# Performance work log

Hardware: AMD Instinct MI355X
Metric: run time of the kernel (lower is better)

## Reference

```python
import jax, jax.numpy as jnp
import numpy as np

N, IN_C, OUT_C, FEAT_C, G = 1_000_000, 64, 64, 128, 4096


def setup_inputs() -> dict:
    key = jax.random.key(0)
    ks = jax.random.split(key, 9)
    x = jax.random.normal(ks[0], (N, IN_C), dtype=jnp.float32)
    origin_feat = jax.random.normal(ks[1], (G, FEAT_C), dtype=jnp.float32)
    latent_point_batch = jax.random.randint(ks[2], (N,), 0, G, dtype=jnp.int32)
    s_fc = 1.0 / np.sqrt(IN_C)
    s_ft = 1.0 / np.sqrt(FEAT_C)
    W_fc = jax.random.uniform(ks[3], (IN_C, OUT_C), jnp.float32, -s_fc, s_fc)
    b_fc = jax.random.uniform(ks[4], (OUT_C,), jnp.float32, -s_fc, s_fc)
    W_mu = jax.random.uniform(ks[5], (FEAT_C, OUT_C), jnp.float32, -s_ft, s_ft)
    b_mu = jax.random.uniform(ks[6], (OUT_C,), jnp.float32, -s_ft, s_ft)
    W_sig = jax.random.uniform(ks[7], (FEAT_C, OUT_C), jnp.float32, -s_ft, s_ft)
    b_sig = jax.random.uniform(ks[8], (OUT_C,), jnp.float32, -s_ft, s_ft)
    return {"x": x, "origin_feat": origin_feat, "latent_point_batch": latent_point_batch,
            "num_groups": G, "W_fc": W_fc, "b_fc": b_fc, "W_mu": W_mu, "b_mu": b_mu,
            "W_sig": W_sig, "b_sig": b_sig}


def _segment_mean(v, seg, num_segments):
    # [N, C] -> [G, C] per-segment mean
    s = jax.ops.segment_sum(v, seg, num_segments=num_segments)
    cnt = jax.ops.segment_sum(jnp.ones((v.shape[0],), v.dtype), seg,
                              num_segments=num_segments)
    return s / jnp.maximum(cnt, 1.0)[:, None]


def reference(x, origin_feat, latent_point_batch, num_groups,
              W_fc, b_fc, W_mu, b_mu, W_sig, b_sig):
    h = x @ W_fc + b_fc                      # [N, outC]
    mu = origin_feat @ W_mu + b_mu           # [G, outC]
    sig = origin_feat @ W_sig + b_sig        # [G, outC]
    seg = latent_point_batch
    h_mean = _segment_mean(h, seg, num_groups)          # [G, outC]
    h_c = h - h_mean[seg]                                # centered
    h_var = _segment_mean(h_c * h_c, seg, num_groups)    # biased var per group
    h_n = h_c / jnp.sqrt(h_var[seg] + 1e-14)
    out = jax.nn.relu(h_n * sig[seg] + mu[seg])
    return out
```

## Files before the change

kernel.cpp:

```cpp
#include <hip/hip_runtime.h>
#include <hip/hip_bf16.h>
#include <stdint.h>

typedef unsigned int u32;
typedef unsigned short u16;

__device__ __forceinline__ float bf2f(u32 b) {
  union { u32 u; float f; } v; v.u = b << 16; return v.f;
}

__global__ void FCAdaINLayer_68719477052_kernel(const u16* __restrict__ xb,
                                                int* __restrict__ cnt, int G,
                                                int* __restrict__ flag) {
  int t = blockIdx.x * blockDim.x + threadIdx.x;
  int stride = gridDim.x * blockDim.x;
  for (int i = t; i < G; i += stride) cnt[i] = 0;
  if (blockIdx.x == 0 && threadIdx.x < 64) {
    int lane = threadIdx.x;
    int big = 0;
    for (int j = lane; j < 2048; j += 64) {
      u32 e = ((u32)xb[j] >> 7) & 0xffu;
      if (e >= 140u) big++;
    }
    unsigned long long m = __ballot(big > 0);
    if (lane == 0) *flag = (__popcll(m) > 8) ? 1 : 0;
  }
}

__global__ void k_hist(const int* __restrict__ lat, int n, int* __restrict__ cnt) {
  int i = blockIdx.x * blockDim.x + threadIdx.x;
  int stride = gridDim.x * blockDim.x;
  for (; i < n; i += stride) atomicAdd(&cnt[lat[i]], 1);
}

__global__ void k_scan(const int* __restrict__ cnt, int G, int* __restrict__ offs,
                       int* __restrict__ cursor) {
  __shared__ int part[256];
  int t = threadIdx.x;
  int per = (G + 255) / 256;
  int base = t * per;
  int s = 0;
  for (int j = 0; j < per; j++) { int g = base + j; if (g < G) s += cnt[g]; }
  part[t] = s;
  __syncthreads();
  if (t == 0) {
    int run = 0;
    for (int j = 0; j < 256; j++) { int v = part[j]; part[j] = run; run += v; }
  }
  __syncthreads();
  int run = part[t];
  for (int j = 0; j < per; j++) {
    int g = base + j;
    if (g < G) { offs[g] = run; cursor[g] = run; run += cnt[g]; }
  }
  if (t == 255) offs[G] = run;
}

__global__ void k_scatter(const int* __restrict__ lat, int n, int* __restrict__ cursor,
                          int* __restrict__ sorted) {
  int i = blockIdx.x * blockDim.x + threadIdx.x;
  int stride = gridDim.x * blockDim.x;
  for (; i < n; i += stride) {
    int g = lat[i];
    int pos = atomicAdd(&cursor[g], 1);
    sorted[pos] = i;
  }
}

template <bool F32>
__global__ void k_musig(const void* __restrict__ of, const void* __restrict__ Wmu,
                        const void* __restrict__ bmu, const void* __restrict__ Wsig,
                        const void* __restrict__ bsig, const int* __restrict__ flag,
                        float* __restrict__ mug, float* __restrict__ sgg, int total) {
  if ((*flag != 0) != F32) return;
  int idx = blockIdx.x * blockDim.x + threadIdx.x;
  if (idx >= total) return;
  int g = idx >> 6, c = idx & 63;
  float a0 = 0.f, a1 = 0.f, bm, bs;
  if (F32) {
    const float* ofr = (const float*)of + (size_t)g * 128;
    const float* wm = (const float*)Wmu;
    const float* wsv = (const float*)Wsig;
    for (int k = 0; k < 128; k++) {
      float ov = ofr[k];
      a0 = fmaf(ov, wm[k * 64 + c], a0);
      a1 = fmaf(ov, wsv[k * 64 + c], a1);
    }
    bm = ((const float*)bmu)[c];
    bs = ((const float*)bsig)[c];
  } else {
    const u16* ofr = (const u16*)of + (size_t)g * 128;
    const u16* wm = (const u16*)Wmu;
    const u16* wsv = (const u16*)Wsig;
    for (int k = 0; k < 128; k++) {
      float ov = bf2f((u32)ofr[k]);
      a0 = fmaf(ov, bf2f((u32)wm[k * 64 + c]), a0);
      a1 = fmaf(ov, bf2f((u32)wsv[k * 64 + c]), a1);
    }
    bm = bf2f((u32)((const u16*)bmu)[c]);
    bs = bf2f((u32)((const u16*)bsig)[c]);
  }
  mug[idx] = a0 + bm;
  sgg[idx] = a1 + bs;
}

__device__ __forceinline__ float h_bf16(const uint4* __restrict__ xr,
                                        const float* wcol, float bc) {
  float h0 = bc, h1 = 0.f, h2 = 0.f, h3 = 0.f;
#pragma unroll
  for (int j = 0; j < 8; j++) {
    uint4 q = xr[j];
    u32 qs[4] = {q.x, q.y, q.z, q.w};
#pragma unroll
    for (int m = 0; m < 4; m++) {
      float flo = __uint_as_float(qs[m] << 16);
      float fhi = __uint_as_float(qs[m] & 0xffff0000u);
      int k = j * 8 + m * 2;
      if ((m & 1) == 0) { h0 = fmaf(flo, wcol[k], h0); h1 = fmaf(fhi, wcol[k + 1], h1); }
      else             { h2 = fmaf(flo, wcol[k], h2); h3 = fmaf(fhi, wcol[k + 1], h3); }
    }
  }
  return (h0 + h2) + (h1 + h3);
}

__device__ __forceinline__ float h_f32(const float4* __restrict__ xr,
                                       const float* wcol, float bc) {
  float h0 = bc, h1 = 0.f, h2 = 0.f, h3 = 0.f;
#pragma unroll
  for (int j = 0; j < 16; j++) {
    float4 q = xr[j];
    int k = j * 4;
    h0 = fmaf(q.x, wcol[k], h0);
    h1 = fmaf(q.y, wcol[k + 1], h1);
    h2 = fmaf(q.z, wcol[k + 2], h2);
    h3 = fmaf(q.w, wcol[k + 3], h3);
  }
  return (h0 + h2) + (h1 + h3);
}

template <bool F32>
__global__ void k_main(const void* __restrict__ x, const int* __restrict__ sorted,
                       const int* __restrict__ offs, const float* __restrict__ mug,
                       const float* __restrict__ sgg, const void* __restrict__ Wfc,
                       const void* __restrict__ bfc, const int* __restrict__ flag,
                       void* __restrict__ out) {
  if ((*flag != 0) != F32) return;
  int g = blockIdx.x;
  int lane = threadIdx.x & 63;
  int wid = threadIdx.x >> 6;
  int beg = offs[g], end = offs[g + 1];
  int cnt = end - beg;
  if (cnt == 0) return;
  __shared__ float red[2][4][64];

  float wcol[64];
  float bc;
  if (F32) {
    const float* W = (const float*)Wfc;
#pragma unroll
    for (int k = 0; k < 64; k++) wcol[k] = W[k * 64 + lane];
    bc = ((const float*)bfc)[lane];
  } else {
    const u16* W = (const u16*)Wfc;
#pragma unroll
    for (int k = 0; k < 64; k++) wcol[k] = bf2f((u32)W[k * 64 + lane]);
    bc = bf2f((u32)((const u16*)bfc)[lane]);
  }

  float ssum = 0.f, ssq = 0.f;
  for (int i = beg + wid; i < end; i += 4) {
    int p = __builtin_amdgcn_readfirstlane(sorted[i]);
    float h;
    if (F32) h = h_f32(reinterpret_cast<const float4*>(x) + (size_t)p * 16, wcol, bc);
    else     h = h_bf16(reinterpret_cast<const uint4*>(x) + (size_t)p * 8, wcol, bc);
    ssum += h;
    ssq = fmaf(h, h, ssq);
  }
  red[0][wid][lane] = ssum;
  red[1][wid][lane] = ssq;
  __syncthreads();
  float ts = 0.f, tq = 0.f;
#pragma unroll
  for (int w = 0; w < 4; w++) { ts += red[0][w][lane]; tq += red[1][w][lane]; }
  float inv = 1.0f / (float)cnt;
  float mean = ts * inv;
  float var = fmaxf(tq * inv - mean * mean, 0.f);
  float rstd = rsqrtf(var + 1e-14f);
  float scale = sgg[(size_t)g * 64 + lane] * rstd;
  float shift = mug[(size_t)g * 64 + lane] - mean * scale;

  for (int i = beg + wid; i < end; i += 4) {
    int p = __builtin_amdgcn_readfirstlane(sorted[i]);
    float h;
    if (F32) h = h_f32(reinterpret_cast<const float4*>(x) + (size_t)p * 16, wcol, bc);
    else     h = h_bf16(reinterpret_cast<const uint4*>(x) + (size_t)p * 8, wcol, bc);
    float o = fmaxf(fmaf(h, scale, shift), 0.f);
    if (F32) ((float*)out)[(size_t)p * 64 + lane] = o;
    else ((__hip_bfloat16*)out)[(size_t)p * 64 + lane] = __float2bfloat16(o);
  }
}

extern "C" void kernel_launch(void* const* d_in, const int* in_sizes, int n_in,
                              void* d_out, int out_size, void* d_ws, size_t ws_size,
                              hipStream_t stream) {
  const void* x   = d_in[0];
  const void* of  = d_in[1];
  const int* lat  = (const int*)d_in[2];
  const void* Wfc = d_in[4];
  const void* bfc = d_in[5];
  const void* Wmu = d_in[6];
  const void* bmu = d_in[7];
  const void* Wsg = d_in[8];
  const void* bsg = d_in[9];

  int N = in_sizes[2];
  int G = in_sizes[1] / 128;

  char* ws = (char*)d_ws;
  size_t o = 0;
  int* flag   = (int*)(ws + o); o += 256;
  int* cnt    = (int*)(ws + o); o += (size_t)G * 4;
  int* offs   = (int*)(ws + o); o += (size_t)(G + 1) * 4;
  int* cursor = (int*)(ws + o); o += (size_t)G * 4;
  o = (o + 255) & ~(size_t)255;
  float* mug  = (float*)(ws + o); o += (size_t)G * 64 * 4;
  float* sgg  = (float*)(ws + o); o += (size_t)G * 64 * 4;
  int* sorted = (int*)(ws + o); o += (size_t)N * 4;

  FCAdaINLayer_68719477052_kernel<<<64, 256, 0, stream>>>((const u16*)x, cnt, G, flag);
  k_hist<<<1024, 256, 0, stream>>>(lat, N, cnt);
  k_scan<<<1, 256, 0, stream>>>(cnt, G, offs, cursor);
  k_scatter<<<1024, 256, 0, stream>>>(lat, N, cursor, sorted);
  k_musig<false><<<(G * 64 + 255) / 256, 256, 0, stream>>>(of, Wmu, bmu, Wsg, bsg, flag, mug, sgg, G * 64);
  k_musig<true><<<(G * 64 + 255) / 256, 256, 0, stream>>>(of, Wmu, bmu, Wsg, bsg, flag, mug, sgg, G * 64);
  k_main<false><<<G, 256, 0, stream>>>(x, sorted, offs, mug, sgg, Wfc, bfc, flag, d_out);
  k_main<true><<<G, 256, 0, stream>>>(x, sorted, offs, mug, sgg, Wfc, bfc, flag, d_out);
}
```

Measured before the change: 1.001 ms.

## Stage group rows in LDS and cache h to avoid second pass recompute

The main kernel now copies up to 312 gathered x rows per group into shared memory, computes h once, and stores h back into the same LDS slot. The normalization pass then reads the cached h instead of reloading x and redoing the 64-wide dot product. The bf16/f32 runtime flag detection and the duplicate kernel launches are removed, leaving a single fp32 path. The cost is about 80KB of LDS per block, which may limit occupancy, and groups larger than 312 rows still fall back to recomputing from global memory.

```diff
diff --git a/kernel.cpp b/kernel.cpp
--- a/kernel.cpp
+++ b/kernel.cpp
@@ -3,28 +3,11 @@
 #include <stdint.h>
 
 typedef unsigned int u32;
-typedef unsigned short u16;
 
-__device__ __forceinline__ float bf2f(u32 b) {
-  union { u32 u; float f; } v; v.u = b << 16; return v.f;
-}
-
-__global__ void FCAdaINLayer_68719477052_kernel(const u16* __restrict__ xb,
-                                                int* __restrict__ cnt, int G,
-                                                int* __restrict__ flag) {
+__global__ void FCAdaINLayer_68719477052_kernel(int* __restrict__ cnt, int G) {
   int t = blockIdx.x * blockDim.x + threadIdx.x;
   int stride = gridDim.x * blockDim.x;
   for (int i = t; i < G; i += stride) cnt[i] = 0;
-  if (blockIdx.x == 0 && threadIdx.x < 64) {
-    int lane = threadIdx.x;
-    int big = 0;
-    for (int j = lane; j < 2048; j += 64) {
-      u32 e = ((u32)xb[j] >> 7) & 0xffu;
-      if (e >= 140u) big++;
-    }
-    unsigned long long m = __ballot(big > 0);
-    if (lane == 0) *flag = (__popcll(m) > 8) ? 1 : 0;
-  }
 }
 
 __global__ void k_hist(const int* __restrict__ lat, int n, int* __restrict__ cnt) {
@@ -67,63 +50,25 @@
   }
 }
 
-template <bool F32>
-__global__ void k_musig(const void* __restrict__ of, const void* __restrict__ Wmu,
-                        const void* __restrict__ bmu, const void* __restrict__ Wsig,
-                        const void* __restrict__ bsig, const int* __restrict__ flag,
-                        float* __restrict__ mug, float* __restrict__ sgg, int total) {
-  if ((*flag != 0) != F32) return;
+__global__ void k_musig(const float* __restrict__ of, const float* __restrict__ Wmu,
+                        const float* __restrict__ bmu, const float* __restrict__ Wsig,
+                        const float* __restrict__ bsig, float* __restrict__ mug,
+                        float* __restrict__ sgg, int total) {
   int idx = blockIdx.x * blockDim.x + threadIdx.x;
   if (idx >= total) return;
   int g = idx >> 6, c = idx & 63;
-  float a0 = 0.f, a1 = 0.f, bm, bs;
-  if (F32) {
-    const float* ofr = (const float*)of + (size_t)g * 128;
-    const float* wm = (const float*)Wmu;
-    const float* wsv = (const float*)Wsig;
-    for (int k = 0; k < 128; k++) {
-      float ov = ofr[k];
-      a0 = fmaf(ov, wm[k * 64 + c], a0);
-      a1 = fmaf(ov, wsv[k * 64 + c], a1);
-    }
-    bm = ((const float*)bmu)[c];
-    bs = ((const float*)bsig)[c];
-  } else {
-    const u16* ofr = (const u16*)of + (size_t)g * 128;
-    const u16* wm = (const u16*)Wmu;
-    const u16* wsv = (const u16*)Wsig;
-    for (int k = 0; k < 128; k++) {
-      float ov = bf2f((u32)ofr[k]);
-      a0 = fmaf(ov, bf2f((u32)wm[k * 64 + c]), a0);
-      a1 = fmaf(ov, bf2f((u32)wsv[k * 64 + c]), a1);
-    }
-    bm = bf2f((u32)((const u16*)bmu)[c]);
-    bs = bf2f((u32)((const u16*)bsig)[c]);
+  const float* ofr = of + (size_t)g * 128;
+  float a0 = 0.f, a1 = 0.f;
+  for (int k = 0; k < 128; k++) {
+    float ov = ofr[k];
+    a0 = fmaf(ov, Wmu[k * 64 + c], a0);
+    a1 = fmaf(ov, Wsig[k * 64 + c], a1);
   }
-  mug[idx] = a0 + bm;
-  sgg[idx] = a1 + bs;
+  mug[idx] = a0 + bmu[c];
+  sgg[idx] = a1 + bsig[c];
 }
 
-__device__ __forceinline__ float h_bf16(const uint4* __restrict__ xr,
-                                        const float* wcol, float bc) {
-  float h0 = bc, h1 = 0.f, h2 = 0.f, h3 = 0.f;
-#pragma unroll
-  for (int j = 0; j < 8; j++) {
-    uint4 q = xr[j];
-    u32 qs[4] = {q.x, q.y, q.z, q.w};
-#pragma unroll
-    for (int m = 0; m < 4; m++) {
-      float flo = __uint_as_float(qs[m] << 16);
-      float fhi = __uint_as_float(qs[m] & 0xffff0000u);
-      int k = j * 8 + m * 2;
-      if ((m & 1) == 0) { h0 = fmaf(flo, wcol[k], h0); h1 = fmaf(fhi, wcol[k + 1], h1); }
-      else             { h2 = fmaf(flo, wcol[k], h2); h3 = fmaf(fhi, wcol[k + 1], h3); }
-    }
-  }
-  return (h0 + h2) + (h1 + h3);
-}
-
-__device__ __forceinline__ float h_f32(const float4* __restrict__ xr,
+__device__ __forceinline__ float dot64(const float4* __restrict__ xr,
                                        const float* wcol, float bc) {
   float h0 = bc, h1 = 0.f, h2 = 0.f, h3 = 0.f;
 #pragma unroll
@@ -138,43 +83,60 @@
   return (h0 + h2) + (h1 + h3);
 }
 
-template <bool F32>
-__global__ void k_main(const void* __restrict__ x, const int* __restrict__ sorted,
-                       const int* __restrict__ offs, const float* __restrict__ mug,
-                       const float* __restrict__ sgg, const void* __restrict__ Wfc,
-                       const void* __restrict__ bfc, const int* __restrict__ flag,
-                       void* __restrict__ out) {
-  if ((*flag != 0) != F32) return;
+#define ROWS 312
+__global__ __launch_bounds__(256) void k_main(
+    const float* __restrict__ x, const int* __restrict__ sorted,
+    const int* __restrict__ offs, const float* __restrict__ mug,
+    const float* __restrict__ sgg, const float* __restrict__ Wfc,
+    const float* __restrict__ bfc, float* __restrict__ out) {
+  __shared__ float xs[ROWS * 64];
+  __shared__ float red[2][4][64];
   int g = blockIdx.x;
-  int lane = threadIdx.x & 63;
-  int wid = threadIdx.x >> 6;
   int beg = offs[g], end = offs[g + 1];
   int cnt = end - beg;
   if (cnt == 0) return;
-  __shared__ float red[2][4][64];
+  int tid = threadIdx.x;
+  int lane = tid & 63, wid = tid >> 6;
+  int rows = cnt < ROWS ? cnt : ROWS;
+
+  for (int idx = tid; idx < rows * 16; idx += 256) {
+    int j = idx >> 4, e = idx & 15;
+    int p = sorted[beg + j];
+    reinterpret_cast<float4*>(xs)[j * 16 + e] =
+        reinterpret_cast<const float4*>(x + (size_t)p * 64)[e];
+  }
+  __syncthreads();
 
   float wcol[64];
-  float bc;
-  if (F32) {
-    const float* W = (const float*)Wfc;
 #pragma unroll
-    for (int k = 0; k < 64; k++) wcol[k] = W[k * 64 + lane];
-    bc = ((const float*)bfc)[lane];
-  } else {
-    const u16* W = (const u16*)Wfc;
-#pragma unroll
-    for (int k = 0; k < 64; k++) wcol[k] = bf2f((u32)W[k * 64 + lane]);
-    bc = bf2f((u32)((const u16*)bfc)[lane]);
-  }
+  for (int k = 0; k < 64; k++) wcol[k] = Wfc[k * 64 + lane];
+  float bc = bfc[lane];
 
   float ssum = 0.f, ssq = 0.f;
-  for (int i = beg + wid; i < end; i += 4) {
-    int p = __builtin_amdgcn_readfirstlane(sorted[i]);
-    float h;
-    if (F32) h = h_f32(reinterpret_cast<const float4*>(x) + (size_t)p * 16, wcol, bc);
-    else     h = h_bf16(reinterpret_cast<const uint4*>(x) + (size_t)p * 8, wcol, bc);
-    ssum += h;
-    ssq = fmaf(h, h, ssq);
+  for (int j = wid; j < cnt; j += 8) {
+    int j2 = j + 4;
+    float h1;
+    if (j < ROWS) {
+      h1 = dot64(reinterpret_cast<const float4*>(xs + j * 64), wcol, bc);
+      xs[j * 64 + lane] = h1;
+    } else {
+      int p = __builtin_amdgcn_readfirstlane(sorted[beg + j]);
+      h1 = dot64(reinterpret_cast<const float4*>(x + (size_t)p * 64), wcol, bc);
+    }
+    ssum += h1;
+    ssq = fmaf(h1, h1, ssq);
+    if (j2 < cnt) {
+      float h2;
+      if (j2 < ROWS) {
+        h2 = dot64(reinterpret_cast<const float4*>(xs + j2 * 64), wcol, bc);
+        xs[j2 * 64 + lane] = h2;
+      } else {
+        int p = __builtin_amdgcn_readfirstlane(sorted[beg + j2]);
+        h2 = dot64(reinterpret_cast<const float4*>(x + (size_t)p * 64), wcol, bc);
+      }
+      ssum += h2;
+      ssq = fmaf(h2, h2, ssq);
+    }
   }
   red[0][wid][lane] = ssum;
   red[1][wid][lane] = ssq;
@@ -189,36 +151,36 @@
   float scale = sgg[(size_t)g * 64 + lane] * rstd;
   float shift = mug[(size_t)g * 64 + lane] - mean * scale;
 
-  for (int i = beg + wid; i < end; i += 4) {
-    int p = __builtin_amdgcn_readfirstlane(sorted[i]);
+  for (int j = wid; j < cnt; j += 4) {
+    int p = __builtin_amdgcn_readfirstlane(sorted[beg + j]);
     float h;
-    if (F32) h = h_f32(reinterpret_cast<const float4*>(x) + (size_t)p * 16, wcol, bc);
-    else     h = h_bf16(reinterpret_cast<const uint4*>(x) + (size_t)p * 8, wcol, bc);
-    float o = fmaxf(fmaf(h, scale, shift), 0.f);
-    if (F32) ((float*)out)[(size_t)p * 64 + lane] = o;
-    else ((__hip_bfloat16*)out)[(size_t)p * 64 + lane] = __float2bfloat16(o);
+    if (j < ROWS) {
+      h = xs[j * 64 + lane];
+    } else {
+      h = dot64(reinterpret_cast<const float4*>(x + (size_t)p * 64), wcol, bc);
+    }
+    out[(size_t)p * 64 + lane] = fmaxf(fmaf(h, scale, shift), 0.f);
   }
 }
 
 extern "C" void kernel_launch(void* const* d_in, const int* in_sizes, int n_in,
                               void* d_out, int out_size, void* d_ws, size_t ws_size,
                               hipStream_t stream) {
-  const void* x   = d_in[0];
-  const void* of  = d_in[1];
-  const int* lat  = (const int*)d_in[2];
-  const void* Wfc = d_in[4];
-  const void* bfc = d_in[5];
-  const void* Wmu = d_in[6];
-  const void* bmu = d_in[7];
-  const void* Wsg = d_in[8];
-  const void* bsg = d_in[9];
+  const float* x   = (const float*)d_in[0];
+  const float* of  = (const float*)d_in[1];
+  const int* lat   = (const int*)d_in[2];
+  const float* Wfc = (const float*)d_in[4];
+  const float* bfc = (const float*)d_in[5];
+  const float* Wmu = (const float*)d_in[6];
+  const float* bmu = (const float*)d_in[7];
+  const float* Wsg = (const float*)d_in[8];
+  const float* bsg = (const float*)d_in[9];
 
   int N = in_sizes[2];
   int G = in_sizes[1] / 128;
 
   char* ws = (char*)d_ws;
   size_t o = 0;
-  int* flag   = (int*)(ws + o); o += 256;
   int* cnt    = (int*)(ws + o); o += (size_t)G * 4;
   int* offs   = (int*)(ws + o); o += (size_t)(G + 1) * 4;
   int* cursor = (int*)(ws + o); o += (size_t)G * 4;
@@ -227,12 +189,10 @@
   float* sgg  = (float*)(ws + o); o += (size_t)G * 64 * 4;
   int* sorted = (int*)(ws + o); o += (size_t)N * 4;
 
-  FCAdaINLayer_68719477052_kernel<<<64, 256, 0, stream>>>((const u16*)x, cnt, G, flag);
+  FCAdaINLayer_68719477052_kernel<<<32, 256, 0, stream>>>(cnt, G);
   k_hist<<<1024, 256, 0, stream>>>(lat, N, cnt);
   k_scan<<<1, 256, 0, stream>>>(cnt, G, offs, cursor);
   k_scatter<<<1024, 256, 0, stream>>>(lat, N, cursor, sorted);
-  k_musig<false><<<(G * 64 + 255) / 256, 256, 0, stream>>>(of, Wmu, bmu, Wsg, bsg, flag, mug, sgg, G * 64);
-  k_musig<true><<<(G * 64 + 255) / 256, 256, 0, stream>>>(of, Wmu, bmu, Wsg, bsg, flag, mug, sgg, G * 64);
-  k_main<false><<<G, 256, 0, stream>>>(x, sorted, offs, mug, sgg, Wfc, bfc, flag, d_out);
-  k_main<true><<<G, 256, 0, stream>>>(x, sorted, offs, mug, sgg, Wfc, bfc, flag, d_out);
+  k_musig<<<(G * 64 + 255) / 256, 256, 0, stream>>>(of, Wmu, bmu, Wsg, bsg, mug, sgg, G * 64);
+  k_main<<<G, 256, 0, stream>>>(x, sorted, offs, mug, sgg, Wfc, bfc, (float*)d_out);
 }
```

Measured after the change: 957.6 us. 4.4% less time.
